# Kernel tuning notes

Measured on AMD Instinct MI355X. Metric: run time of the kernel, lower is better.

## Reference

```python
import jax, jax.numpy as jnp
import numpy as np

H, W = 256, 256
N = 512
BG = jnp.zeros(3, dtype=jnp.float32)  # background_color=(0,0,0)


def setup_inputs() -> dict:
    key = jax.random.key(0)
    k1, k2, k3, k4, k5 = jax.random.split(key, 5)
    # positions: xy in [-1.5,1.5], z in [2,6] so every gaussian passes the z>0.01 test
    xy = jax.random.uniform(k1, (N, 2), minval=-1.5, maxval=1.5, dtype=jnp.float32)
    zpos = jax.random.uniform(k2, (N, 1), minval=2.0, maxval=6.0, dtype=jnp.float32)
    positions = jnp.concatenate([xy, zpos], axis=-1)
    # PSD 3D covariances with ~0.05 world-space std
    A = 0.05 * jax.random.normal(k3, (N, 3, 3), dtype=jnp.float32)
    cov3d = A @ jnp.swapaxes(A, -1, -2) + 1e-6 * jnp.eye(3, dtype=jnp.float32)
    opacities = jax.random.uniform(k4, (N, 1), dtype=jnp.float32)
    colors = jax.random.uniform(k5, (N, 3), dtype=jnp.float32)
    K = jnp.array([[300.0, 0.0, 128.0], [0.0, 300.0, 128.0], [0.0, 0.0, 1.0]], dtype=jnp.float32)
    R = jnp.eye(3, dtype=jnp.float32)
    t = jnp.zeros(3, dtype=jnp.float32)
    return {"positions": positions, "cov3d": cov3d, "opacities": opacities,
            "colors": colors, "K": K, "R": R, "t": t}


def _render(positions, cov3d, opacities, colors, K, R, t):
    # --- project means to camera / image space ---
    means_cam = positions @ R.T + t                       # (N,3)
    z = means_cam[:, 2]                                   # all > 0.01 by construction
    proj = means_cam @ K.T                                # (N,3)
    means_2d = proj[:, :2] / proj[:, 2:3]                 # (N,2) pixel coords (x,y)

    # --- project 3D covariance to 2D: cov2d = J (R cov3d R^T) J^T + 0.3 I ---
    fx, fy = K[0, 0], K[1, 1]
    xc, yc = means_cam[:, 0], means_cam[:, 1]
    zero = jnp.zeros_like(z)
    J = jnp.stack([
        jnp.stack([fx / z, zero, -fx * xc / z**2], axis=-1),
        jnp.stack([zero, fy / z, -fy * yc / z**2], axis=-1),
    ], axis=1)                                            # (N,2,3)
    cov_cam = jnp.einsum('ij,njk,lk->nil', R, cov3d, R)   # (N,3,3)
    cov2d = jnp.einsum('nij,njk,nlk->nil', J, cov_cam, J) + 0.3 * jnp.eye(2, dtype=jnp.float32)

    # --- front-to-back depth sort ---
    order = jnp.argsort(z)
    means_2d = means_2d[order]
    cov2d = cov2d[order]
    opac = opacities[:, 0][order]
    cols = colors[order]

    # --- 2x2 inverse and 3-sigma radii ---
    a, b, c = cov2d[:, 0, 0], cov2d[:, 0, 1], cov2d[:, 1, 1]
    det = jnp.clip(a * c - b * b, 1e-8, None)
    inv00, inv01, inv11 = c / det, -b / det, a / det
    max_eig = (a + c) * 0.5 + jnp.sqrt(jnp.clip(((a - c) * 0.5) ** 2 + b ** 2, 1e-8, None))
    radii = 3.0 * jnp.sqrt(max_eig)

    # --- bounding boxes (int() truncates toward zero, as in torch) ---
    mx, my = means_2d[:, 0], means_2d[:, 1]
    x_min = jnp.maximum(0.0, jnp.trunc(mx - radii))
    x_max = jnp.minimum(float(W), jnp.trunc(mx + radii) + 1.0)
    y_min = jnp.maximum(0.0, jnp.trunc(my - radii))
    y_max = jnp.minimum(float(H), jnp.trunc(my + radii) + 1.0)

    xs = jnp.arange(W, dtype=jnp.float32)
    ys = jnp.arange(H, dtype=jnp.float32)
    dx = xs[None, :] - mx[:, None]                        # (N,W)
    dy = ys[None, :] - my[:, None]                        # (N,H)
    mask_x = (xs[None, :] >= x_min[:, None]) & (xs[None, :] < x_max[:, None])
    mask_y = (ys[None, :] >= y_min[:, None]) & (ys[None, :] < y_max[:, None])
    mask = (mask_y[:, :, None] & mask_x[:, None, :]).astype(jnp.float32)  # (N,H,W)

    # --- gaussian weights on the grid ---
    mahal = (inv00[:, None, None] * dx[:, None, :] ** 2
             + 2.0 * inv01[:, None, None] * dy[:, :, None] * dx[:, None, :]
             + inv11[:, None, None] * dy[:, :, None] ** 2)                 # (N,H,W)
    alpha = opac[:, None, None] * jnp.exp(-0.5 * mahal) * mask            # (N,H,W)

    # --- front-to-back alpha compositing ---
    # sequential: contrib_i = alpha_i * (1 - alpha_acc_{i-1}); alpha_acc_i += contrib_i
    # closed form: T_i = prod_{j<i} (1 - alpha_j)  (exclusive cumprod)
    T = jnp.concatenate([jnp.ones((1, H, W), dtype=alpha.dtype),
                         jnp.cumprod(1.0 - alpha, axis=0)[:-1]], axis=0)
    contrib = alpha * T                                                   # (N,H,W)
    image = BG[None, None, :] + jnp.einsum('nhw,nc->hwc', contrib, cols)  # (H,W,3)
    return image


def reference(positions, cov3d, opacities, colors, K, R, t):
    return _render(positions, cov3d, opacities, colors, K, R, t)
```

## Files before the change

### kernel.cpp

```cpp
#include <hip/hip_runtime.h>


constexpr int IMG_H = 256;
constexpr int IMG_W = 256;
constexpr int MAXN  = 512;
constexpr int TW    = 16;
constexpr int TH    = 16;
constexpr int NTHR  = TW * TH;

__global__ __launch_bounds__(NTHR) void fused_raster_kernel(
    const float* __restrict__ positions,
    const float* __restrict__ cov3d,
    const float* __restrict__ opacities,
    const float* __restrict__ colors,
    const float* __restrict__ Km,
    const float* __restrict__ Rm,
    const float* __restrict__ tv,
    float* __restrict__ out)
{
    __shared__ float4 s_all[MAXN * 4];
    __shared__ float  s_z[MAXN];
    __shared__ int    s_list[MAXN];
    __shared__ int    s_order[MAXN];
    __shared__ unsigned long long s_mask[8];
    __shared__ int    s_cnt[8];
    __shared__ int    s_total;

    const int tid  = threadIdx.y * TW + threadIdx.x;
    const int lane = tid & 63;
    const int wv   = tid >> 6;

    const float tx0 = (float)(blockIdx.x * TW);
    const float ty0 = (float)(blockIdx.y * TH);

    const float R00 = Rm[0], R01 = Rm[1], R02 = Rm[2];
    const float R10 = Rm[3], R11 = Rm[4], R12 = Rm[5];
    const float R20 = Rm[6], R21 = Rm[7], R22 = Rm[8];
    const float t0 = tv[0], t1 = tv[1], t2 = tv[2];
    const float K00 = Km[0], K01 = Km[1], K02 = Km[2];
    const float K10 = Km[3], K11 = Km[4], K12 = Km[5];
    const float K20 = Km[6], K21 = Km[7], K22 = Km[8];
    const float fx = K00, fy = K11;

    #pragma unroll
    for (int k = 0; k < 2; ++k) {
        const int g = k * NTHR + tid;

        const float px = positions[g*3+0];
        const float py = positions[g*3+1];
        const float pz = positions[g*3+2];

        const float cx = R00*px + R01*py + R02*pz + t0;
        const float cy = R10*px + R11*py + R12*pz + t1;
        const float cz = R20*px + R21*py + R22*pz + t2;

        const float pr0 = K00*cx + K01*cy + K02*cz;
        const float pr1 = K10*cx + K11*cy + K12*cz;
        const float pr2 = K20*cx + K21*cy + K22*cz;
        const float mx = pr0 / pr2;
        const float my = pr1 / pr2;

        const float invz  = 1.0f / cz;
        const float invz2 = invz * invz;
        const float j00 =  fx * invz;
        const float j02 = -fx * cx * invz2;
        const float j11 =  fy * invz;
        const float j12 = -fy * cy * invz2;

        const float C00 = cov3d[g*9+0], C01 = cov3d[g*9+1], C02 = cov3d[g*9+2];
        const float C10 = cov3d[g*9+3], C11 = cov3d[g*9+4], C12 = cov3d[g*9+5];
        const float C20 = cov3d[g*9+6], C21 = cov3d[g*9+7], C22 = cov3d[g*9+8];

        const float T100 = R00*C00 + R01*C10 + R02*C20;
        const float T101 = R00*C01 + R01*C11 + R02*C21;
        const float T102 = R00*C02 + R01*C12 + R02*C22;
        const float T110 = R10*C00 + R11*C10 + R12*C20;
        const float T111 = R10*C01 + R11*C11 + R12*C21;
        const float T112 = R10*C02 + R11*C12 + R12*C22;
        const float T120 = R20*C00 + R21*C10 + R22*C20;
        const float T121 = R20*C01 + R21*C11 + R22*C21;
        const float T122 = R20*C02 + R21*C12 + R22*C22;
        const float M00 = T100*R00 + T101*R01 + T102*R02;
        const float M01 = T100*R10 + T101*R11 + T102*R12;
        const float M02 = T100*R20 + T101*R21 + T102*R22;
        const float M11 = T110*R10 + T111*R11 + T112*R12;
        const float M12 = T110*R20 + T111*R21 + T112*R22;
        const float M20 = T120*R00 + T121*R01 + T122*R02;
        const float M21 = T120*R10 + T121*R11 + T122*R12;
        const float M22 = T120*R20 + T121*R21 + T122*R22;

        const float v00 = M00*j00 + M02*j02;
        const float v02 = M20*j00 + M22*j02;
        const float v10 = M01*j11 + M02*j12;
        const float v11 = M11*j11 + M12*j12;
        const float v12 = M21*j11 + M22*j12;

        const float va = j00*v00 + j02*v02 + 0.3f;
        const float vb = j00*v10 + j02*v12;
        const float vc = j11*v11 + j12*v12 + 0.3f;

        const float det  = fmaxf(va*vc - vb*vb, 1e-8f);
        const float idet = 1.0f / det;
        const float inv00 =  vc * idet;
        const float inv01 = -vb * idet;
        const float inv11 =  va * idet;

        const float half_diff = (va - vc) * 0.5f;
        const float disc = fmaxf(half_diff*half_diff + vb*vb, 1e-8f);
        const float max_eig = (va + vc) * 0.5f + sqrtf(disc);
        const float radii = 3.0f * sqrtf(max_eig);

        const float x_min = fmaxf(0.0f, truncf(mx - radii));
        const float x_max = fminf((float)IMG_W, truncf(mx + radii) + 1.0f);
        const float y_min = fmaxf(0.0f, truncf(my - radii));
        const float y_max = fminf((float)IMG_H, truncf(my + radii) + 1.0f);

        s_all[g*4+0] = make_float4(x_min, x_max, y_min, y_max);
        s_all[g*4+1] = make_float4(mx, my, -0.5f*inv00, -inv01);
        s_all[g*4+2] = make_float4(-0.5f*inv11, opacities[g],
                                   colors[g*3+0], colors[g*3+1]);
        s_all[g*4+3] = make_float4(colors[g*3+2], 0.0f, 0.0f, 0.0f);
        s_z[g] = cz;

        const bool hit = (x_min < tx0 + (float)TW) && (x_max > tx0) &&
                         (y_min < ty0 + (float)TH) && (y_max > ty0);
        const unsigned long long m = __ballot(hit);
        if (lane == 0) {
            const int seg = 4*k + wv;
            s_mask[seg] = m;
            s_cnt[seg]  = __popcll(m);
        }
    }
    __syncthreads();

    #pragma unroll
    for (int k = 0; k < 2; ++k) {
        const int seg = 4*k + wv;
        int base = 0;
        #pragma unroll
        for (int q = 0; q < 8; ++q) base += (q < seg) ? s_cnt[q] : 0;
        const unsigned long long m = s_mask[seg];
        if ((m >> lane) & 1ull) {
            const int pos = base + __popcll(m & ((1ull << lane) - 1ull));
            s_list[pos] = seg * 64 + lane;
        }
    }
    if (tid == 0) {
        int t = 0;
        #pragma unroll
        for (int q = 0; q < 8; ++q) t += s_cnt[q];
        s_total = t;
    }
    __syncthreads();
    const int K = s_total;

    for (int m = tid; m < K; m += NTHR) {
        const int   g  = s_list[m];
        const float zg = s_z[g];
        int rank = 0;
        for (int j = 0; j < K; ++j) {
            const int   gj = s_list[j];
            const float zj = s_z[gj];
            rank += (zj < zg || (zj == zg && gj < g)) ? 1 : 0;
        }
        s_order[rank] = g;
    }
    __syncthreads();

    const int x = blockIdx.x * TW + threadIdx.x;
    const int y = blockIdx.y * TH + threadIdx.y;
    const float fxp = (float)x;
    const float fyp = (float)y;

    float T = 1.0f, accr = 0.0f, accg = 0.0f, accb = 0.0f;
    for (int m = 0; m < K; ++m) {
        const int g = s_order[m];
        const float4 bb = s_all[g*4+0];
        const float4 p1 = s_all[g*4+1];
        const float4 p2 = s_all[g*4+2];
        const float  cb = s_all[g*4+3].x;
        const bool in = (fxp >= bb.x) & (fxp < bb.y) & (fyp >= bb.z) & (fyp < bb.w);
        const float dx = fxp - p1.x;
        const float dy = fyp - p1.y;
        const float e = p1.z*dx*dx + p1.w*dx*dy + p2.x*dy*dy;
        const float a = in ? p2.y * __expf(e) : 0.0f;
        const float w = T * a;
        accr = fmaf(w, p2.z, accr);
        accg = fmaf(w, p2.w, accg);
        accb = fmaf(w, cb, accb);
        T *= (1.0f - a);
    }

    const int pix = (y * IMG_W + x) * 3;
    out[pix + 0] = accr;
    out[pix + 1] = accg;
    out[pix + 2] = accb;
}

extern "C" void kernel_launch(void* const* d_in, const int* in_sizes, int n_in,
                              void* d_out, int out_size, void* d_ws, size_t ws_size,
                              hipStream_t stream)
{
    const float* positions = (const float*)d_in[0];
    const float* cov3d     = (const float*)d_in[1];
    const float* opacities = (const float*)d_in[2];
    const float* colors    = (const float*)d_in[3];
    const float* Km        = (const float*)d_in[4];
    const float* Rm        = (const float*)d_in[5];
    const float* tv        = (const float*)d_in[6];
    float* out = (float*)d_out;

    dim3 block(TW, TH);
    dim3 grid(IMG_W / TW, IMG_H / TH);
    fused_raster_kernel<<<grid, block, 0, stream>>>(
        positions, cov3d, opacities, colors, Km, Rm, tv, out);
}
```

Before: 79.61 us.

## Sort packed z-index keys in registers, store sorted gaussians, early-exit compositing

Per-tile culling now appends packed (depth bits, index) 64-bit keys via a shared atomic counter, and each thread computes the rank of its own gaussians, replacing the ballot/prefix compaction and the strided rank loop. Gaussian parameters are written directly in depth order, with tile-local bounding boxes packed into one word, so the compositing loop reads contiguous data without indirection. The loop processes two gaussians per iteration with software prefetch and exits once every lane's transmittance falls below a small threshold. The early exit drops contributions below 1e-5 and so slightly departs from the exact reference.

```diff
diff --git a/kernel.cpp b/kernel.cpp
--- a/kernel.cpp
+++ b/kernel.cpp
@@ -18,20 +18,17 @@
     const float* __restrict__ tv,
     float* __restrict__ out)
 {
-    __shared__ float4 s_all[MAXN * 4];
-    __shared__ float  s_z[MAXN];
-    __shared__ int    s_list[MAXN];
-    __shared__ int    s_order[MAXN];
-    __shared__ unsigned long long s_mask[8];
-    __shared__ int    s_cnt[8];
-    __shared__ int    s_total;
-
-    const int tid  = threadIdx.y * TW + threadIdx.x;
-    const int lane = tid & 63;
-    const int wv   = tid >> 6;
-
-    const float tx0 = (float)(blockIdx.x * TW);
-    const float ty0 = (float)(blockIdx.y * TH);
+    __shared__ float4 s_srt[(MAXN + 4) * 3];
+    __shared__ unsigned long long s_key[MAXN];
+    __shared__ int s_total;
+
+    const int tid = threadIdx.y * TW + threadIdx.x;
+    if (tid == 0) s_total = 0;
+
+    const int tx0i = blockIdx.x * TW;
+    const int ty0i = blockIdx.y * TH;
+    const float tx0 = (float)tx0i;
+    const float ty0 = (float)ty0i;
 
     const float R00 = Rm[0], R01 = Rm[1], R02 = Rm[2];
     const float R10 = Rm[3], R11 = Rm[4], R12 = Rm[5];
@@ -41,6 +38,14 @@
     const float K10 = Km[3], K11 = Km[4], K12 = Km[5];
     const float K20 = Km[6], K21 = Km[7], K22 = Km[8];
     const float fx = K00, fy = K11;
+
+    __syncthreads();
+
+    float r_mx[2], r_my[2], r_h00[2], r_h01[2], r_h11[2];
+    float r_op[2], r_cr[2], r_cg[2], r_cb[2];
+    float r_xmin[2], r_xmax[2], r_ymin[2], r_ymax[2];
+    unsigned long long r_key[2];
+    bool r_hit[2];
 
     #pragma unroll
     for (int k = 0; k < 2; ++k) {
@@ -115,83 +120,101 @@
         const float y_min = fmaxf(0.0f, truncf(my - radii));
         const float y_max = fminf((float)IMG_H, truncf(my + radii) + 1.0f);
 
-        s_all[g*4+0] = make_float4(x_min, x_max, y_min, y_max);
-        s_all[g*4+1] = make_float4(mx, my, -0.5f*inv00, -inv01);
-        s_all[g*4+2] = make_float4(-0.5f*inv11, opacities[g],
-                                   colors[g*3+0], colors[g*3+1]);
-        s_all[g*4+3] = make_float4(colors[g*3+2], 0.0f, 0.0f, 0.0f);
-        s_z[g] = cz;
+        r_mx[k] = mx;  r_my[k] = my;
+        r_h00[k] = -0.5f*inv00;  r_h01[k] = -inv01;  r_h11[k] = -0.5f*inv11;
+        r_op[k] = opacities[g];
+        r_cr[k] = colors[g*3+0]; r_cg[k] = colors[g*3+1]; r_cb[k] = colors[g*3+2];
+        r_xmin[k] = x_min; r_xmax[k] = x_max;
+        r_ymin[k] = y_min; r_ymax[k] = y_max;
+
+        r_key[k] = ((unsigned long long)__float_as_uint(cz) << 32) | (unsigned)g;
 
         const bool hit = (x_min < tx0 + (float)TW) && (x_max > tx0) &&
                          (y_min < ty0 + (float)TH) && (y_max > ty0);
-        const unsigned long long m = __ballot(hit);
-        if (lane == 0) {
-            const int seg = 4*k + wv;
-            s_mask[seg] = m;
-            s_cnt[seg]  = __popcll(m);
+        r_hit[k] = hit;
+        if (hit) {
+            const int pos = atomicAdd(&s_total, 1);
+            s_key[pos] = r_key[k];
         }
     }
     __syncthreads();
+    const int K = s_total;
+
+    int rank0 = 0, rank1 = 0;
+    for (int j = 0; j < K; ++j) {
+        const unsigned long long kj = s_key[j];
+        rank0 += (kj < r_key[0]) ? 1 : 0;
+        rank1 += (kj < r_key[1]) ? 1 : 0;
+    }
 
     #pragma unroll
     for (int k = 0; k < 2; ++k) {
-        const int seg = 4*k + wv;
-        int base = 0;
-        #pragma unroll
-        for (int q = 0; q < 8; ++q) base += (q < seg) ? s_cnt[q] : 0;
-        const unsigned long long m = s_mask[seg];
-        if ((m >> lane) & 1ull) {
-            const int pos = base + __popcll(m & ((1ull << lane) - 1ull));
-            s_list[pos] = seg * 64 + lane;
-        }
-    }
-    if (tid == 0) {
-        int t = 0;
-        #pragma unroll
-        for (int q = 0; q < 8; ++q) t += s_cnt[q];
-        s_total = t;
-    }
+        if (r_hit[k]) {
+            const int xm = max(0,  (int)r_xmin[k] - tx0i);
+            const int xM = min(TW, (int)r_xmax[k] - tx0i);
+            const int ym = max(0,  (int)r_ymin[k] - ty0i);
+            const int yM = min(TH, (int)r_ymax[k] - ty0i);
+            const unsigned pk = (unsigned)xm | ((unsigned)xM << 5)
+                              | ((unsigned)ym << 10) | ((unsigned)yM << 15);
+            const int rk = (k == 0) ? rank0 : rank1;
+            s_srt[rk*3+0] = make_float4(r_mx[k], r_my[k], r_h00[k], r_h01[k]);
+            s_srt[rk*3+1] = make_float4(r_h11[k], r_op[k], r_cr[k], r_cg[k]);
+            s_srt[rk*3+2] = make_float4(r_cb[k], __uint_as_float(pk), 0.0f, 0.0f);
+        }
+    }
+    if (tid < 6) s_srt[K*3 + tid] = make_float4(0.0f, 0.0f, 0.0f, 0.0f);
     __syncthreads();
-    const int K = s_total;
-
-    for (int m = tid; m < K; m += NTHR) {
-        const int   g  = s_list[m];
-        const float zg = s_z[g];
-        int rank = 0;
-        for (int j = 0; j < K; ++j) {
-            const int   gj = s_list[j];
-            const float zj = s_z[gj];
-            rank += (zj < zg || (zj == zg && gj < g)) ? 1 : 0;
-        }
-        s_order[rank] = g;
-    }
-    __syncthreads();
-
-    const int x = blockIdx.x * TW + threadIdx.x;
-    const int y = blockIdx.y * TH + threadIdx.y;
-    const float fxp = (float)x;
-    const float fyp = (float)y;
+
+    const int tix = threadIdx.x, tiy = threadIdx.y;
+    const float fxp = (float)(tx0i + tix);
+    const float fyp = (float)(ty0i + tiy);
 
     float T = 1.0f, accr = 0.0f, accg = 0.0f, accb = 0.0f;
-    for (int m = 0; m < K; ++m) {
-        const int g = s_order[m];
-        const float4 bb = s_all[g*4+0];
-        const float4 p1 = s_all[g*4+1];
-        const float4 p2 = s_all[g*4+2];
-        const float  cb = s_all[g*4+3].x;
-        const bool in = (fxp >= bb.x) & (fxp < bb.y) & (fyp >= bb.z) & (fyp < bb.w);
-        const float dx = fxp - p1.x;
-        const float dy = fyp - p1.y;
-        const float e = p1.z*dx*dx + p1.w*dx*dy + p2.x*dy*dy;
-        const float a = in ? p2.y * __expf(e) : 0.0f;
-        const float w = T * a;
-        accr = fmaf(w, p2.z, accr);
-        accg = fmaf(w, p2.w, accg);
-        accb = fmaf(w, cb, accb);
-        T *= (1.0f - a);
-    }
-
-    const int pix = (y * IMG_W + x) * 3;
+
+    float4 A0 = s_srt[0], A1 = s_srt[1], A2 = s_srt[2];
+    float4 B0 = s_srt[3], B1 = s_srt[4], B2 = s_srt[5];
+
+    for (int m = 0; m < K; m += 2) {
+        const int pf = (m + 2) * 3;
+        const float4 C0 = s_srt[pf+0], C1 = s_srt[pf+1], C2 = s_srt[pf+2];
+        const float4 D0 = s_srt[pf+3], D1 = s_srt[pf+4], D2 = s_srt[pf+5];
+
+        {
+            const unsigned pk = __float_as_uint(A2.y);
+            const bool in = (tix >= (int)(pk & 31u)) & (tix < (int)((pk >> 5) & 31u))
+                          & (tiy >= (int)((pk >> 10) & 31u)) & (tiy < (int)((pk >> 15) & 31u));
+            const float dx = fxp - A0.x;
+            const float dy = fyp - A0.y;
+            const float e = A0.z*dx*dx + A0.w*dx*dy + A1.x*dy*dy;
+            const float a = in ? A1.y * __expf(e) : 0.0f;
+            const float w = T * a;
+            accr = fmaf(w, A1.z, accr);
+            accg = fmaf(w, A1.w, accg);
+            accb = fmaf(w, A2.x, accb);
+            T *= (1.0f - a);
+        }
+        {
+            const unsigned pk = __float_as_uint(B2.y);
+            const bool in = (tix >= (int)(pk & 31u)) & (tix < (int)((pk >> 5) & 31u))
+                          & (tiy >= (int)((pk >> 10) & 31u)) & (tiy < (int)((pk >> 15) & 31u));
+            const float dx = fxp - B0.x;
+            const float dy = fyp - B0.y;
+            const float e = B0.z*dx*dx + B0.w*dx*dy + B1.x*dy*dy;
+            const float a = in ? B1.y * __expf(e) : 0.0f;
+            const float w = T * a;
+            accr = fmaf(w, B1.z, accr);
+            accg = fmaf(w, B1.w, accg);
+            accb = fmaf(w, B2.x, accb);
+            T *= (1.0f - a);
+        }
+
+        A0 = C0; A1 = C1; A2 = C2;
+        B0 = D0; B1 = D1; B2 = D2;
+
+        if (!__any(T > 1.0e-5f)) break;
+    }
+
+    const int pix = ((ty0i + tiy) * IMG_W + (tx0i + tix)) * 3;
     out[pix + 0] = accr;
     out[pix + 1] = accg;
     out[pix + 2] = accb;
```

Measured after the change: 76.39 us. 4.0% less time.
